# Kernel tuning notes

Hardware: AMD Instinct MI355X
Metric: run time of the kernel (lower is better)

Reference implementation:

```python
import jax, jax.numpy as jnp
import numpy as np

T = 16384      # total packed tokens
C = 1024       # d_model
H = 16         # n_head
HD = C // H    # head dim = 64
N_SEG = 32     # number of equal varlen segments
SEG = T // N_SEG


def setup_inputs() -> dict:
    key = jax.random.key(0)
    k1, k2, k3 = jax.random.split(key, 3)
    x = jax.random.normal(k1, (T, C), dtype=jnp.float32)
    w_attn = jax.random.normal(k2, (C, 3 * C), dtype=jnp.float32) * (1.0 / np.sqrt(C))
    w_proj = jax.random.normal(k3, (C, C), dtype=jnp.float32) * (1.0 / np.sqrt(C))
    # boundary indices for torch.tensor_split -> 32 equal segments of SEG tokens
    split_sections = (jnp.arange(1, N_SEG) * SEG).astype(jnp.int64)
    return {"x": x, "w_attn": w_attn, "w_proj": w_proj, "split_sections": split_sections}


def reference(x, w_attn, w_proj, split_sections):
    # x: [T, C] packed tokens; split_sections: 31 boundaries -> 32 equal segments
    n_seg = int(np.asarray(split_sections).shape[0]) + 1
    seg = x.shape[0] // n_seg
    qkv = x @ w_attn                                   # [T, 3C]
    q, k, v = jnp.split(qkv, 3, axis=-1)               # each [T, C]

    def heads(t):
        # [T, C] -> [H, n_seg, seg, HD]  (block-diagonal segment layout)
        return t.reshape(x.shape[0], H, HD).transpose(1, 0, 2).reshape(H, n_seg, seg, HD)

    q, k, v = heads(q), heads(k), heads(v)
    scale = 1.0 / np.sqrt(HD)
    att = jnp.einsum('hnqd,hnkd->hnqk', q, k) * scale  # [H, n_seg, seg, seg]
    att = jax.nn.softmax(att, axis=-1)
    y = jnp.einsum('hnqk,hnkd->hnqd', att, v)          # [H, n_seg, seg, HD]
    y = y.reshape(H, x.shape[0], HD).transpose(1, 0, 2).reshape(x.shape[0], C)
    return y @ w_proj                                  # [T, C]
```

## Files before the change

### kernel.cpp

```cpp
#include <hip/hip_runtime.h>
#include <hip/hip_bf16.h>
#include <stdint.h>

typedef __attribute__((ext_vector_type(8))) short short8;
typedef __attribute__((ext_vector_type(4))) short short4_t;
typedef __attribute__((ext_vector_type(4))) float float4_t;

#define GLOAD_LDS16(gp, lp)                                                              \
  __builtin_amdgcn_global_load_lds((const __attribute__((address_space(1))) unsigned int*)(gp), \
                                   (__attribute__((address_space(3))) unsigned int*)(lp), \
                                   16, 0, 0)

__device__ __forceinline__ float4_t mfma_bf16(short8 a, short8 b, float4_t c) {
  return __builtin_amdgcn_mfma_f32_16x16x32_bf16(a, b, c, 0, 0, 0);
}

__device__ __forceinline__ short f2bf(float f) {
  union { float f; unsigned int u; } v; v.f = f;
  unsigned int r = v.u + 0x7fff + ((v.u >> 16) & 1);
  return (short)(r >> 16);
}

__device__ __forceinline__ float red_sum16(float v) {
  v += __shfl_xor(v, 1);
  v += __shfl_xor(v, 2);
  v += __shfl_xor(v, 4);
  v += __shfl_xor(v, 8);
  return v;
}

__device__ __forceinline__ long swz_col(long colbase64, int chunk, int sub, int row) {
  return colbase64 + ((chunk ^ (row & 7)) << 3) + sub;
}

__global__ __launch_bounds__(256) void conv_swz(const float* __restrict__ in,
                                                short* __restrict__ out, long nchunks) {
  for (long ch = (long)blockIdx.x * blockDim.x + threadIdx.x; ch < nchunks;
       ch += (long)gridDim.x * blockDim.x) {
    long r  = ch >> 7;
    int cir = (int)(ch & 127);
    int pc  = (cir & ~3) | ((cir & 3) ^ (((int)r >> 1) & 3));
    const float* src = in + ch * 8;
    short8 o;
#pragma unroll
    for (int j = 0; j < 8; ++j) o[j] = f2bf(src[j]);
    *(short8*)&out[r * 1024 + pc * 8] = o;
  }
}

__global__ __launch_bounds__(256) void transpose_conv(const float* __restrict__ in,
                                                      short* __restrict__ out,
                                                      int R, int C) {
  __shared__ short tile[32][33];
  int c0 = blockIdx.x * 32;
  int r0 = blockIdx.y * 32;
  int tx = threadIdx.x;
  int ty = threadIdx.y;
#pragma unroll
  for (int i = 0; i < 4; ++i)
    tile[ty + i * 8][tx] = f2bf(in[(long)(r0 + ty + i * 8) * C + c0 + tx]);
  __syncthreads();
#pragma unroll
  for (int i = 0; i < 4; ++i) {
    int n   = c0 + ty + i * 8;
    long cc = (long)r0 + ((((tx >> 3) ^ ((n >> 1) & 3))) << 3) + (tx & 7);
    out[(long)n * R + cc] = tile[tx][ty + i * 8];
  }
}

template <int MODE>
__global__ __launch_bounds__(512, 2) void gemm256(const short* __restrict__ A, long lda,
                                                  const short* __restrict__ Bt, long ldb,
                                                  void* __restrict__ Cv,
                                                  short* __restrict__ vT,
                                                  int M, int N, int K) {
  __shared__ __align__(16) short As[4][256 * 32];
  __shared__ __align__(16) short Bs[4][256 * 32];

  const int tid  = threadIdx.x;
  const int wave = tid >> 6;
  const int lane = tid & 63;
  const int rA   = lane & 15;
  const int q4   = lane >> 4;
  const int wm   = (wave >> 2) * 128;
  const int wn   = (wave & 3) * 64;

  const int nbx = N >> 8;
  const int nwg = nbx * (M >> 8);
  const int bid = (int)blockIdx.y * nbx + (int)blockIdx.x;
  const int cpx = nwg >> 3;
  const int swz = (bid & 7) * cpx + (bid >> 3);
  const long m0 = (long)(swz / nbx) * 256;
  const long n0 = (long)(swz % nbx) * 256;

  const short* Ag = A  + (m0 + (tid >> 2)) * lda + (tid & 3) * 8;
  const short* Bg = Bt + (n0 + (tid >> 2)) * ldb + (tid & 3) * 8;

#define STAGE_A(u)                                                          \
  {                                                                         \
    const int slot_ = (u) & 3;                                              \
    GLOAD_LDS16(Ag + (u) * 32,             &As[slot_][wave * 512]);         \
    GLOAD_LDS16(Ag + 128 * lda + (u) * 32, &As[slot_][4096 + wave * 512]);  \
  }
#define STAGE_B(u)                                                          \
  {                                                                         \
    const int slot_ = (u) & 3;                                              \
    GLOAD_LDS16(Bg + (u) * 32,             &Bs[slot_][wave * 512]);         \
    GLOAD_LDS16(Bg + 128 * ldb + (u) * 32, &Bs[slot_][4096 + wave * 512]);  \
  }

  float4_t acc[8][4];
#pragma unroll
  for (int i = 0; i < 8; ++i)
#pragma unroll
    for (int j = 0; j < 4; ++j) acc[i][j] = (float4_t){0.f, 0.f, 0.f, 0.f};

  const int nt = K >> 5;
  const int cswz = q4 ^ ((rA >> 1) & 3);

  STAGE_A(0); STAGE_B(0);
  STAGE_A(1); STAGE_B(1);
  STAGE_A(2); STAGE_B(2);
  asm volatile("s_waitcnt vmcnt(8)" ::: "memory");
  __builtin_amdgcn_s_barrier();

  short8 afl[4], afh[4], bf0[4], bf1[4];
#pragma unroll
  for (int mi = 0; mi < 4; ++mi)
    afl[mi] = *(const short8*)&As[0][((wm + mi * 16 + rA) * 4 + cswz) * 8];
#pragma unroll
  for (int ni = 0; ni < 4; ++ni)
    bf0[ni] = *(const short8*)&Bs[0][((wn + ni * 16 + rA) * 4 + cswz) * 8];

  auto tile_step = [&](int u, short8 (&bc)[4], short8 (&bn)[4]) {
    const int slot = u & 3;
#pragma unroll
    for (int mi = 0; mi < 4; ++mi)
      afh[mi] = *(const short8*)&As[slot][((wm + 64 + mi * 16 + rA) * 4 + cswz) * 8];
    if (u + 3 < nt) STAGE_A(u + 3);
    asm volatile("s_waitcnt lgkmcnt(4)" ::: "memory");
    __builtin_amdgcn_s_setprio(1);
#pragma unroll
    for (int mi = 0; mi < 4; ++mi)
#pragma unroll
      for (int ni = 0; ni < 4; ++ni)
        acc[mi][ni] = mfma_bf16(afl[mi], bc[ni], acc[mi][ni]);
    __builtin_amdgcn_s_setprio(0);
    if (u + 3 < nt)      asm volatile("s_waitcnt vmcnt(6)" ::: "memory");
    else if (u + 2 < nt) asm volatile("s_waitcnt vmcnt(4)" ::: "memory");
    else                 asm volatile("s_waitcnt vmcnt(0)" ::: "memory");
    __builtin_amdgcn_s_barrier();
    if (u + 1 < nt) {
      const int ns = (u + 1) & 3;
#pragma unroll
      for (int mi = 0; mi < 4; ++mi)
        afl[mi] = *(const short8*)&As[ns][((wm + mi * 16 + rA) * 4 + cswz) * 8];
#pragma unroll
      for (int ni = 0; ni < 4; ++ni)
        bn[ni] = *(const short8*)&Bs[ns][((wn + ni * 16 + rA) * 4 + cswz) * 8];
    }
    if (u + 3 < nt) STAGE_B(u + 3);
    if (u + 1 < nt) asm volatile("s_waitcnt lgkmcnt(8)" ::: "memory");
    else            asm volatile("s_waitcnt lgkmcnt(0)" ::: "memory");
    __builtin_amdgcn_s_setprio(1);
#pragma unroll
    for (int mi = 0; mi < 4; ++mi)
#pragma unroll
      for (int ni = 0; ni < 4; ++ni)
        acc[mi + 4][ni] = mfma_bf16(afh[mi], bc[ni], acc[mi + 4][ni]);
    __builtin_amdgcn_s_setprio(0);
    __builtin_amdgcn_s_barrier();
  };

  for (int u = 0; u < nt; u += 2) {
    tile_step(u,     bf0, bf1);
    tile_step(u + 1, bf1, bf0);
  }
#undef STAGE_A
#undef STAGE_B

  if constexpr (MODE == 1) {
    short* Cq = (short*)Cv;
    if (n0 >= 2048) {
#pragma unroll
      for (int mi = 0; mi < 8; ++mi) {
        int tbase = (int)m0 + wm + mi * 16 + q4 * 4;
        int ct    = (tbase >> 3) & 7;
#pragma unroll
        for (int ni = 0; ni < 4; ++ni) {
          int c = (int)n0 + wn + ni * 16 + rA;
          int d = c - 2048;
          long dst = (long)d * 16384 + (tbase & ~63) +
                     (((ct ^ (d & 7))) << 3) + (tbase & 7);
          short4_t o;
#pragma unroll
          for (int reg = 0; reg < 4; ++reg) o[reg] = f2bf(acc[mi][ni][reg]);
          *(short4_t*)&vT[dst] = o;
        }
      }
    } else {
#pragma unroll
      for (int mi = 0; mi < 8; ++mi)
#pragma unroll
        for (int ni = 0; ni < 4; ++ni)
#pragma unroll
          for (int reg = 0; reg < 4; ++reg) {
            long t = m0 + wm + mi * 16 + q4 * 4 + reg;
            int  c = (int)n0 + wn + ni * 16 + rA;
            long cc = swz_col((long)(c & ~63), (c >> 3) & 7, c & 7, (int)t);
            Cq[t * 3072 + cc] = f2bf(acc[mi][ni][reg]);
          }
    }
  } else {
    float* Co = (float*)Cv;
    (void)vT;
#pragma unroll
    for (int mi = 0; mi < 8; ++mi)
#pragma unroll
      for (int ni = 0; ni < 4; ++ni)
#pragma unroll
        for (int reg = 0; reg < 4; ++reg) {
          long row = m0 + wm + mi * 16 + q4 * 4 + reg;
          long col = n0 + wn + ni * 16 + rA;
          Co[row * (long)N + col] = acc[mi][ni][reg];
        }
  }
}

__global__ __launch_bounds__(256, 2) void attn_kernel(short* __restrict__ qkv,
                                                      const short* __restrict__ vT) {
  __shared__ __align__(16) short Qs[128 * 64];
  __shared__ __align__(16) short Ks[2][64 * 64];
  __shared__ __align__(16) short Vt[2][64 * 64];
  __shared__ __align__(16) short Ps[128 * 72];

  const int tid  = threadIdx.x;
  const int wave = tid >> 6;
  const int lane = tid & 63;
  const int rA   = lane & 15;
  const int q4   = lane >> 4;
  const int qt   = blockIdx.x;
  const int seg  = blockIdx.y;
  const int h    = blockIdx.z;

  const long tq0  = (long)seg * 512 + qt * 128;
  const long tk0  = (long)seg * 512;
  const long hoff = (long)h * 64;

#pragma unroll
  for (int i = 0; i < 4; ++i) {
    int slot = i * 256 + tid;
    int r    = slot >> 3;
    int c    = slot & 7;
    GLOAD_LDS16(qkv + (tq0 + r) * 3072 + hoff + c * 8, &Qs[(i * 256 + wave * 64) * 8]);
  }
#pragma unroll
  for (int i = 0; i < 2; ++i) {
    int slot = i * 256 + tid;
    int r    = slot >> 3;
    int c    = slot & 7;
    GLOAD_LDS16(qkv + (tk0 + r) * 3072 + 1024 + hoff + c * 8,
                &Ks[0][(i * 256 + wave * 64) * 8]);
    GLOAD_LDS16(vT + (hoff + r) * 16384 + tk0 + c * 8,
                &Vt[0][(i * 256 + wave * 64) * 8]);
  }

  float4_t acc_o[2][4];
  float l_st[2][4];
#pragma unroll
  for (int mi = 0; mi < 2; ++mi)
#pragma unroll
    for (int di = 0; di < 4; ++di) acc_o[mi][di] = (float4_t){0.f, 0.f, 0.f, 0.f};
#pragma unroll
  for (int mi = 0; mi < 2; ++mi)
#pragma unroll
    for (int reg = 0; reg < 4; ++reg) l_st[mi][reg] = 0.f;

  for (int kt = 0; kt < 8; ++kt) {
    const int p = kt & 1;
    __syncthreads();

    if (kt < 7) {
      const long tkn = tk0 + (kt + 1) * 64;
#pragma unroll
      for (int i = 0; i < 2; ++i) {
        int slot = i * 256 + tid;
        int r    = slot >> 3;
        int c    = slot & 7;
        GLOAD_LDS16(qkv + (tkn + r) * 3072 + 1024 + hoff + c * 8,
                    &Ks[1 - p][(i * 256 + wave * 64) * 8]);
        GLOAD_LDS16(vT + (hoff + r) * 16384 + tkn + c * 8,
                    &Vt[1 - p][(i * 256 + wave * 64) * 8]);
      }
    }

    float4_t s_acc[2][4];
#pragma unroll
    for (int mi = 0; mi < 2; ++mi)
#pragma unroll
      for (int ni = 0; ni < 4; ++ni) s_acc[mi][ni] = (float4_t){0.f, 0.f, 0.f, 0.f};
#pragma unroll
    for (int kk = 0; kk < 2; ++kk) {
      int cp = (kk * 4 + q4) ^ (rA & 7);
      short8 af[2], bfr[4];
#pragma unroll
      for (int mi = 0; mi < 2; ++mi) {
        int r  = wave * 32 + mi * 16 + rA;
        af[mi] = *(const short8*)&Qs[(r * 8 + cp) * 8];
      }
#pragma unroll
      for (int ni = 0; ni < 4; ++ni) {
        int r  = ni * 16 + rA;
        bfr[ni] = *(const short8*)&Ks[p][(r * 8 + cp) * 8];
      }
#pragma unroll
      for (int mi = 0; mi < 2; ++mi)
#pragma unroll
        for (int ni = 0; ni < 4; ++ni)
          s_acc[mi][ni] = mfma_bf16(af[mi], bfr[ni], s_acc[mi][ni]);
    }

#pragma unroll
    for (int mi = 0; mi < 2; ++mi)
#pragma unroll
      for (int reg = 0; reg < 4; ++reg) {
        float rs = 0.f;
#pragma unroll
        for (int ni = 0; ni < 4; ++ni) {
          float pv = __expf(s_acc[mi][ni][reg] * 0.125f);
          s_acc[mi][ni][reg] = pv;
          rs += pv;
        }
        l_st[mi][reg] += rs;
      }

#pragma unroll
    for (int mi = 0; mi < 2; ++mi)
#pragma unroll
      for (int ni = 0; ni < 4; ++ni)
#pragma unroll
        for (int reg = 0; reg < 4; ++reg)
          Ps[(wave * 32 + mi * 16 + q4 * 4 + reg) * 72 + ni * 16 + rA] =
              f2bf(s_acc[mi][ni][reg]);

    __syncthreads();

#pragma unroll
    for (int kk = 0; kk < 2; ++kk) {
      int cp = (kk * 4 + q4) ^ (rA & 7);
      short8 af[2], bfr[4];
#pragma unroll
      for (int mi = 0; mi < 2; ++mi)
        af[mi] = *(const short8*)&Ps[(wave * 32 + mi * 16 + rA) * 72 + (kk * 4 + q4) * 8];
#pragma unroll
      for (int di = 0; di < 4; ++di)
        bfr[di] = *(const short8*)&Vt[p][((di * 16 + rA) * 8 + cp) * 8];
#pragma unroll
      for (int mi = 0; mi < 2; ++mi)
#pragma unroll
        for (int di = 0; di < 4; ++di)
          acc_o[mi][di] = mfma_bf16(af[mi], bfr[di], acc_o[mi][di]);
    }
  }

#pragma unroll
  for (int mi = 0; mi < 2; ++mi)
#pragma unroll
    for (int reg = 0; reg < 4; ++reg) {
      float l  = red_sum16(l_st[mi][reg]);
      float rl = 1.0f / l;
      long t = tq0 + wave * 32 + mi * 16 + q4 * 4 + reg;
#pragma unroll
      for (int di = 0; di < 4; ++di) {
        int c  = di * 16 + rA;
        long cc = hoff + (c & 32) +
                  (((((c >> 3) & 3) ^ (((int)t >> 1) & 3))) << 3) + (c & 7);
        qkv[t * 3072 + cc] = f2bf(acc_o[mi][di][reg] * rl);
      }
    }
}

extern "C" void kernel_launch(void* const* d_in, const int* in_sizes, int n_in,
                              void* d_out, int out_size, void* d_ws, size_t ws_size,
                              hipStream_t stream) {
  const float* x      = (const float*)d_in[0];
  const float* w_attn = (const float*)d_in[1];
  const float* w_proj = (const float*)d_in[2];
  float* out = (float*)d_out;

  short* wT_a = (short*)d_ws;
  short* wT_p = wT_a + (size_t)3072 * 1024;
  short* qkv  = wT_p + (size_t)1024 * 1024;

  short* xb = (short*)d_out;
  short* vT = xb + (size_t)16384 * 1024;

  conv_swz<<<2048, 256, 0, stream>>>(x, xb, (long)16384 * 1024 / 8);
  transpose_conv<<<dim3(3072 / 32, 1024 / 32), dim3(32, 8), 0, stream>>>(w_attn, wT_a, 1024, 3072);
  transpose_conv<<<dim3(1024 / 32, 1024 / 32), dim3(32, 8), 0, stream>>>(w_proj, wT_p, 1024, 1024);

  gemm256<1><<<dim3(3072 / 256, 16384 / 256), 512, 0, stream>>>(xb, 1024, wT_a, 1024, qkv, vT,
                                                                16384, 3072, 1024);

  attn_kernel<<<dim3(4, 32, 16), 256, 0, stream>>>(qkv, vT);

  gemm256<2><<<dim3(1024 / 256, 16384 / 256), 512, 0, stream>>>(qkv, 3072, wT_p, 1024, out, nullptr,
                                                                16384, 1024, 1024);
}
```

Baseline: 353.0 us.

## Replace QKV GEMM with simpler 128x128 tile kernel using 64-wide XOR swizzle

The QKV projection now uses a new gemm_bt kernel with 128x128 tiles, 256 threads and a single-buffered K=64 loop that loads through global_load_lds. To match it, the x and w_attn conversion kernels switch to an 8-way XOR swizzle over 64-element rows. The old pipelined 256x256 gemm256 is kept only for the output projection. The new kernel gives up the multi-stage prefetch and priority scheduling of gemm256 in exchange for a smaller tile and more blocks, so it may expose more load latency.

```diff
diff --git a/kernel.cpp b/kernel.cpp
--- a/kernel.cpp
+++ b/kernel.cpp
@@ -39,7 +39,7 @@
        ch += (long)gridDim.x * blockDim.x) {
     long r  = ch >> 7;
     int cir = (int)(ch & 127);
-    int pc  = (cir & ~3) | ((cir & 3) ^ (((int)r >> 1) & 3));
+    int pc  = (cir & ~7) | ((cir & 7) ^ ((int)r & 7));
     const float* src = in + ch * 8;
     short8 o;
 #pragma unroll
@@ -48,6 +48,7 @@
   }
 }
 
+template <int SWZ64>
 __global__ __launch_bounds__(256) void transpose_conv(const float* __restrict__ in,
                                                       short* __restrict__ out,
                                                       int R, int C) {
@@ -63,16 +64,111 @@
 #pragma unroll
   for (int i = 0; i < 4; ++i) {
     int n   = c0 + ty + i * 8;
-    long cc = (long)r0 + ((((tx >> 3) ^ ((n >> 1) & 3))) << 3) + (tx & 7);
+    int col = r0 + tx;
+    long cc;
+    if constexpr (SWZ64) {
+      cc = swz_col((long)(col & ~63), (col >> 3) & 7, col & 7, n);
+    } else {
+      cc = (long)r0 + ((((tx >> 3) ^ ((n >> 1) & 3))) << 3) + (tx & 7);
+    }
     out[(long)n * R + cc] = tile[tx][ty + i * 8];
   }
 }
 
-template <int MODE>
+__global__ __launch_bounds__(256, 2) void gemm_bt(const short* __restrict__ A, long lda,
+                                                  const short* __restrict__ Bt,
+                                                  short* __restrict__ Cq,
+                                                  short* __restrict__ vT,
+                                                  int M, int N, int K) {
+  __shared__ __align__(16) short As[128 * 64];
+  __shared__ __align__(16) short Bs[128 * 64];
+
+  const int tid  = threadIdx.x;
+  const int wave = tid >> 6;
+  const int lane = tid & 63;
+  const int rA   = lane & 15;
+  const int q4   = lane >> 4;
+  const long m0  = (long)blockIdx.y * 128;
+  const long n0  = (long)blockIdx.x * 128;
+  const int wm   = (wave & 1) * 64;
+  const int wn   = (wave >> 1) * 64;
+
+  float4_t acc[4][4];
+#pragma unroll
+  for (int i = 0; i < 4; ++i)
+#pragma unroll
+    for (int j = 0; j < 4; ++j) acc[i][j] = (float4_t){0.f, 0.f, 0.f, 0.f};
+
+  for (int k0 = 0; k0 < K; k0 += 64) {
+#pragma unroll
+    for (int i = 0; i < 4; ++i) {
+      int slot = i * 256 + tid;
+      int r    = slot >> 3;
+      int c    = slot & 7;
+      const short* ga = A  + (m0 + r) * lda      + k0 + c * 8;
+      const short* gb = Bt + (n0 + r) * (long)K  + k0 + c * 8;
+      GLOAD_LDS16(ga, &As[(i * 256 + wave * 64) * 8]);
+      GLOAD_LDS16(gb, &Bs[(i * 256 + wave * 64) * 8]);
+    }
+    __syncthreads();
+#pragma unroll
+    for (int kk = 0; kk < 2; ++kk) {
+      int cp = (kk * 4 + q4) ^ (rA & 7);
+      short8 af[4], bfr[4];
+#pragma unroll
+      for (int mi = 0; mi < 4; ++mi) {
+        int r  = wm + mi * 16 + rA;
+        af[mi] = *(const short8*)&As[(r * 8 + cp) * 8];
+      }
+#pragma unroll
+      for (int ni = 0; ni < 4; ++ni) {
+        int r  = wn + ni * 16 + rA;
+        bfr[ni] = *(const short8*)&Bs[(r * 8 + cp) * 8];
+      }
+#pragma unroll
+      for (int mi = 0; mi < 4; ++mi)
+#pragma unroll
+        for (int ni = 0; ni < 4; ++ni)
+          acc[mi][ni] = mfma_bf16(af[mi], bfr[ni], acc[mi][ni]);
+    }
+    __syncthreads();
+  }
+
+  if (n0 >= 2048) {
+#pragma unroll
+    for (int mi = 0; mi < 4; ++mi) {
+      int tbase = (int)m0 + wm + mi * 16 + q4 * 4;
+      int ct    = (tbase >> 3) & 7;
+#pragma unroll
+      for (int ni = 0; ni < 4; ++ni) {
+        int c = (int)n0 + wn + ni * 16 + rA;
+        int d = c - 2048;
+        long dst = (long)d * 16384 + (long)(tbase & ~63) +
+                   (((ct ^ (d & 7))) << 3) + (tbase & 7);
+        short4_t o;
+#pragma unroll
+        for (int reg = 0; reg < 4; ++reg) o[reg] = f2bf(acc[mi][ni][reg]);
+        *(short4_t*)&vT[dst] = o;
+      }
+    }
+  } else {
+#pragma unroll
+    for (int mi = 0; mi < 4; ++mi)
+#pragma unroll
+      for (int ni = 0; ni < 4; ++ni)
+#pragma unroll
+        for (int reg = 0; reg < 4; ++reg) {
+          long t = m0 + wm + mi * 16 + q4 * 4 + reg;
+          int  c = (int)n0 + wn + ni * 16 + rA;
+          long cc = swz_col((long)(c & ~63), (c >> 3) & 7, c & 7, (int)t);
+          Cq[t * 3072 + cc] = f2bf(acc[mi][ni][reg]);
+        }
+  }
+}
+
 __global__ __launch_bounds__(512, 2) void gemm256(const short* __restrict__ A, long lda,
                                                   const short* __restrict__ Bt, long ldb,
-                                                  void* __restrict__ Cv,
-                                                  short* __restrict__ vT,
+                                                  float* __restrict__ Co,
                                                   int M, int N, int K) {
   __shared__ __align__(16) short As[4][256 * 32];
   __shared__ __align__(16) short Bs[4][256 * 32];
@@ -179,52 +275,16 @@
 #undef STAGE_A
 #undef STAGE_B
 
-  if constexpr (MODE == 1) {
-    short* Cq = (short*)Cv;
-    if (n0 >= 2048) {
-#pragma unroll
-      for (int mi = 0; mi < 8; ++mi) {
-        int tbase = (int)m0 + wm + mi * 16 + q4 * 4;
-        int ct    = (tbase >> 3) & 7;
-#pragma unroll
-        for (int ni = 0; ni < 4; ++ni) {
-          int c = (int)n0 + wn + ni * 16 + rA;
-          int d = c - 2048;
-          long dst = (long)d * 16384 + (tbase & ~63) +
-                     (((ct ^ (d & 7))) << 3) + (tbase & 7);
-          short4_t o;
-#pragma unroll
-          for (int reg = 0; reg < 4; ++reg) o[reg] = f2bf(acc[mi][ni][reg]);
-          *(short4_t*)&vT[dst] = o;
-        }
-      }
-    } else {
-#pragma unroll
-      for (int mi = 0; mi < 8; ++mi)
-#pragma unroll
-        for (int ni = 0; ni < 4; ++ni)
-#pragma unroll
-          for (int reg = 0; reg < 4; ++reg) {
-            long t = m0 + wm + mi * 16 + q4 * 4 + reg;
-            int  c = (int)n0 + wn + ni * 16 + rA;
-            long cc = swz_col((long)(c & ~63), (c >> 3) & 7, c & 7, (int)t);
-            Cq[t * 3072 + cc] = f2bf(acc[mi][ni][reg]);
-          }
-    }
-  } else {
-    float* Co = (float*)Cv;
-    (void)vT;
-#pragma unroll
-    for (int mi = 0; mi < 8; ++mi)
-#pragma unroll
-      for (int ni = 0; ni < 4; ++ni)
-#pragma unroll
-        for (int reg = 0; reg < 4; ++reg) {
-          long row = m0 + wm + mi * 16 + q4 * 4 + reg;
-          long col = n0 + wn + ni * 16 + rA;
-          Co[row * (long)N + col] = acc[mi][ni][reg];
-        }
-  }
+#pragma unroll
+  for (int mi = 0; mi < 8; ++mi)
+#pragma unroll
+    for (int ni = 0; ni < 4; ++ni)
+#pragma unroll
+      for (int reg = 0; reg < 4; ++reg) {
+        long row = m0 + wm + mi * 16 + q4 * 4 + reg;
+        long col = n0 + wn + ni * 16 + rA;
+        Co[row * (long)N + col] = acc[mi][ni][reg];
+      }
 }
 
 __global__ __launch_bounds__(256, 2) void attn_kernel(short* __restrict__ qkv,
@@ -396,14 +456,14 @@
   short* vT = xb + (size_t)16384 * 1024;
 
   conv_swz<<<2048, 256, 0, stream>>>(x, xb, (long)16384 * 1024 / 8);
-  transpose_conv<<<dim3(3072 / 32, 1024 / 32), dim3(32, 8), 0, stream>>>(w_attn, wT_a, 1024, 3072);
-  transpose_conv<<<dim3(1024 / 32, 1024 / 32), dim3(32, 8), 0, stream>>>(w_proj, wT_p, 1024, 1024);
-
-  gemm256<1><<<dim3(3072 / 256, 16384 / 256), 512, 0, stream>>>(xb, 1024, wT_a, 1024, qkv, vT,
-                                                                16384, 3072, 1024);
+  transpose_conv<1><<<dim3(3072 / 32, 1024 / 32), dim3(32, 8), 0, stream>>>(w_attn, wT_a, 1024, 3072);
+  transpose_conv<0><<<dim3(1024 / 32, 1024 / 32), dim3(32, 8), 0, stream>>>(w_proj, wT_p, 1024, 1024);
+
+  gemm_bt<<<dim3(3072 / 128, 16384 / 128), 256, 0, stream>>>(xb, 1024, wT_a, qkv, vT,
+                                                             16384, 3072, 1024);
 
   attn_kernel<<<dim3(4, 32, 16), 256, 0, stream>>>(qkv, vT);
 
-  gemm256<2><<<dim3(1024 / 256, 16384 / 256), 512, 0, stream>>>(qkv, 3072, wT_p, 1024, out, nullptr,
-                                                                16384, 1024, 1024);
-}
+  gemm256<<<dim3(1024 / 256, 16384 / 256), 512, 0, stream>>>(qkv, 3072, wT_p, 1024, out,
+                                                             16384, 1024, 1024);
+}
```

Result: no change. 357.3 us (+1.2%).
